# Kernel tuning notes

Measured on AMD Instinct MI355X. Metric: run time of the kernel, lower is better.

Reference implementation:

```python
import jax, jax.numpy as jnp
import numpy as np

N_NODES = 100000
N_EDGES = 1600000
D = 256
N_QUERY = 50000

def setup_inputs() -> dict:
    key = jax.random.key(0)
    k1, k2, k3, k4, k5, k6 = jax.random.split(key, 6)
    embeddings = jax.random.normal(k1, (N_NODES, D), dtype=jnp.float32)
    edge_src = jax.random.randint(k2, (N_EDGES,), 0, N_NODES)
    edge_dst = jax.random.randint(k3, (N_EDGES,), 0, N_NODES)
    edge_w = jax.random.uniform(k4, (N_EDGES,), dtype=jnp.float32)
    node_ids = jax.random.randint(k5, (N_QUERY,), 0, N_NODES)
    # Xavier-uniform linear weight, zero bias (as in _init_weights)
    limit = float(np.sqrt(6.0 / (D + D)))
    W = jax.random.uniform(k6, (D, D), dtype=jnp.float32, minval=-limit, maxval=limit)
    b = jnp.zeros((D,), dtype=jnp.float32)
    return {"embeddings": embeddings, "edge_src": edge_src, "edge_dst": edge_dst,
            "edge_w": edge_w, "node_ids": node_ids, "W": W, "b": b}

def reference(embeddings, edge_src, edge_dst, edge_w, node_ids, W, b):
    # graph_convolution: sparse adj (COO) @ embeddings == scatter-add of weighted src rows into dst
    msgs = embeddings[edge_src] * edge_w[:, None]                # [E, D]
    agg = jax.ops.segment_sum(msgs, edge_dst, num_segments=N_NODES)  # [N, D]
    # predict_scores: gather queried nodes, apply linear classifier
    feats = agg[node_ids]                                        # [Q, D]
    return feats @ W.T + b                                       # [Q, D]
```

## Files before the change

kernel.cpp:

```cpp
#include <hip/hip_runtime.h>

#define D 256
#define TQ 32
#define GQ 64

typedef __attribute__((ext_vector_type(8))) short short8;
typedef __attribute__((ext_vector_type(4))) float f32x4;

__device__ __forceinline__ unsigned short f2bf(float x) {
    unsigned int u = __float_as_uint(x);
    unsigned int r = (u + 0x7FFFu + ((u >> 16) & 1u)) >> 16;
    return (unsigned short)r;
}


__global__ __launch_bounds__(256) void flag_kernel(
    const int* __restrict__ nid, unsigned char* __restrict__ flags, int Q)
{
    int q = blockIdx.x * 256 + threadIdx.x;
    if (q < Q) flags[nid[q]] = 1;
}

__global__ __launch_bounds__(256) void hist_kernel(
    const int* __restrict__ edst, const unsigned char* __restrict__ flags,
    int* __restrict__ counts, int E)
{
    int stride = gridDim.x * 256;
    for (int e = blockIdx.x * 256 + threadIdx.x; e < E; e += stride) {
        int d = edst[e];
        if (flags[d]) atomicAdd(&counts[d], 1);
    }
}

__global__ __launch_bounds__(256) void alloc_kernel(
    const int* __restrict__ counts, int* __restrict__ base,
    int* __restrict__ pos, int* __restrict__ total, int N)
{
    int n = blockIdx.x * 256 + threadIdx.x;
    if (n >= N) return;
    int c = counts[n];
    int b = 0;
    if (c > 0) b = atomicAdd(total, c);
    base[n] = b;
    pos[n]  = b;
}

__global__ __launch_bounds__(256) void bucket_kernel(
    const int* __restrict__ esrc, const int* __restrict__ edst,
    const float* __restrict__ ew, const unsigned char* __restrict__ flags,
    int* __restrict__ pos, int2* __restrict__ bucket, int E)
{
    int stride = gridDim.x * 256;
    for (int e = blockIdx.x * 256 + threadIdx.x; e < E; e += stride) {
        int d = edst[e];
        if (flags[d]) {
            int idx = atomicAdd(&pos[d], 1);
            bucket[idx] = make_int2(esrc[e], __float_as_int(ew[e]));
        }
    }
}

__global__ __launch_bounds__(256) void accum_nodes(
    const float4* __restrict__ emb,
    const int2*   __restrict__ bucket,
    const int*    __restrict__ base,
    const int*    __restrict__ counts,
    const unsigned char* __restrict__ flags,
    float4*       __restrict__ agg,
    int N)
{
    const int lane = threadIdx.x & 63;
    const int wid  = (int)((blockIdx.x * 256 + threadIdx.x) >> 6);
    if (wid >= N) return;
    if (!flags[wid]) return;

    const int b = base[wid];
    const int c = counts[wid];
    float4 acc = make_float4(0.f, 0.f, 0.f, 0.f);

    int i = 0;
    for (; i + 4 <= c; i += 4) {
        int2 s0 = bucket[b + i + 0];
        int2 s1 = bucket[b + i + 1];
        int2 s2 = bucket[b + i + 2];
        int2 s3 = bucket[b + i + 3];
        float4 v0 = emb[(size_t)s0.x * (D / 4) + lane];
        float4 v1 = emb[(size_t)s1.x * (D / 4) + lane];
        float4 v2 = emb[(size_t)s2.x * (D / 4) + lane];
        float4 v3 = emb[(size_t)s3.x * (D / 4) + lane];
        float w0 = __int_as_float(s0.y), w1 = __int_as_float(s1.y);
        float w2 = __int_as_float(s2.y), w3 = __int_as_float(s3.y);
        acc.x += v0.x * w0; acc.y += v0.y * w0; acc.z += v0.z * w0; acc.w += v0.w * w0;
        acc.x += v1.x * w1; acc.y += v1.y * w1; acc.z += v1.z * w1; acc.w += v1.w * w1;
        acc.x += v2.x * w2; acc.y += v2.y * w2; acc.z += v2.z * w2; acc.w += v2.w * w2;
        acc.x += v3.x * w3; acc.y += v3.y * w3; acc.z += v3.z * w3; acc.w += v3.w * w3;
    }
    for (; i < c; ++i) {
        int2 s = bucket[b + i];
        float4 v = emb[(size_t)s.x * (D / 4) + lane];
        float w = __int_as_float(s.y);
        acc.x += v.x * w; acc.y += v.y * w; acc.z += v.z * w; acc.w += v.w * w;
    }
    agg[(size_t)wid * (D / 4) + lane] = acc;
}


__global__ __launch_bounds__(256) void scatter_edges(
    const float4* __restrict__ emb, const int* __restrict__ esrc,
    const int* __restrict__ edst, const float* __restrict__ ew,
    float* __restrict__ agg, int E)
{
    const int lane = threadIdx.x & 63;
    const int wid  = (int)((blockIdx.x * blockDim.x + threadIdx.x) >> 6);
    const int nw   = (int)((gridDim.x * blockDim.x) >> 6);
    for (int e = wid; e < E; e += nw) {
        const int   s = esrc[e];
        const int   d = edst[e];
        const float w = ew[e];
        float4 v = emb[(size_t)s * (D / 4) + lane];
        float* o = agg + (size_t)d * D + lane * 4;
        unsafeAtomicAdd(o + 0, v.x * w);
        unsafeAtomicAdd(o + 1, v.y * w);
        unsafeAtomicAdd(o + 2, v.z * w);
        unsafeAtomicAdd(o + 3, v.w * w);
    }
}

__global__ __launch_bounds__(256) void convert_w(
    const float* __restrict__ W, unsigned short* __restrict__ Wbf)
{
    int i = blockIdx.x * 256 + threadIdx.x;
    const float4* src = (const float4*)W + (size_t)i * 2;
    float4 v0 = src[0];
    float4 v1 = src[1];
    short8 p;
    p[0] = (short)f2bf(v0.x); p[1] = (short)f2bf(v0.y);
    p[2] = (short)f2bf(v0.z); p[3] = (short)f2bf(v0.w);
    p[4] = (short)f2bf(v1.x); p[5] = (short)f2bf(v1.y);
    p[6] = (short)f2bf(v1.z); p[7] = (short)f2bf(v1.w);
    *((short8*)Wbf + i) = p;
}

__global__ __launch_bounds__(256) void gather_gemm_mfma(
    const float* __restrict__ agg, const int* __restrict__ nid,
    const unsigned short* __restrict__ Wbf,
    const float* __restrict__ b,
    float* __restrict__ out, int Q)
{
    __shared__ unsigned char lds[GQ * 512];
    const int t  = threadIdx.x;
    const int q0 = blockIdx.x * GQ;

    #pragma unroll
    for (int s = 0; s < 8; ++s) {
        const int i   = t + s * 256;
        const int row = i >> 5;
        const int ch  = i & 31;
        const int q   = q0 + row;
        float4 v0 = make_float4(0.f, 0.f, 0.f, 0.f), v1 = v0;
        if (q < Q) {
            const float4* src = (const float4*)agg + (size_t)nid[q] * 64 + ch * 2;
            v0 = src[0];
            v1 = src[1];
        }
        short8 p;
        p[0] = (short)f2bf(v0.x); p[1] = (short)f2bf(v0.y);
        p[2] = (short)f2bf(v0.z); p[3] = (short)f2bf(v0.w);
        p[4] = (short)f2bf(v1.x); p[5] = (short)f2bf(v1.y);
        p[6] = (short)f2bf(v1.z); p[7] = (short)f2bf(v1.w);
        int byte = row * 512 + ch * 16;
        byte ^= (row & 7) << 4;
        *(short8*)(lds + byte) = p;
    }
    __syncthreads();

    const int wave = t >> 6;
    const int lane = t & 63;
    const int qw   = wave * 16;
    const int lrow = lane & 15;
    const int kg   = lane >> 4;

    short8 afrag[8];
    #pragma unroll
    for (int ks = 0; ks < 8; ++ks) {
        int byte = (qw + lrow) * 512 + ks * 64 + kg * 16;
        byte ^= ((qw + lrow) & 7) << 4;
        afrag[ks] = *(const short8*)(lds + byte);
    }

    const unsigned short* wp0 = Wbf + (size_t)lrow * 256 + kg * 8;

    for (int jt = 0; jt < 16; ++jt) {
        f32x4 acc = {0.f, 0.f, 0.f, 0.f};
        const unsigned short* wp = wp0 + (size_t)jt * 16 * 256;
        #pragma unroll
        for (int ks = 0; ks < 8; ++ks) {
            short8 bfrag = *(const short8*)(wp + ks * 32);
            acc = __builtin_amdgcn_mfma_f32_16x16x32_bf16(afrag[ks], bfrag, acc, 0, 0, 0);
        }
        const float bias = b[jt * 16 + lrow];
        #pragma unroll
        for (int r = 0; r < 4; ++r) {
            const int row = kg * 4 + r;
            const int q   = q0 + qw + row;
            if (q < Q) out[(size_t)q * D + jt * 16 + lrow] = acc[r] + bias;
        }
    }
}

__global__ __launch_bounds__(256) void gather_gemm_w(
    const float* __restrict__ agg, const int* __restrict__ nid,
    const float* __restrict__ W, const float* __restrict__ b,
    float* __restrict__ out, int Q)
{
    __shared__ float fl[TQ][D];
    const int t  = threadIdx.x;
    const int q0 = blockIdx.x * TQ;

    for (int i = t; i < TQ * (D / 4); i += 256) {
        const int r = i >> 6;
        const int c = i & 63;
        const int q = q0 + r;
        float4 v = make_float4(0.f, 0.f, 0.f, 0.f);
        if (q < Q) v = ((const float4*)agg)[(size_t)nid[q] * (D / 4) + c];
        ((float4*)&fl[r][0])[c] = v;
    }
    __syncthreads();

    const int j = t;
    float acc[TQ];
    #pragma unroll
    for (int r = 0; r < TQ; ++r) acc[r] = 0.f;

    const float4* wr4 = (const float4*)(W + (size_t)j * D);
    for (int k4 = 0; k4 < D / 4; ++k4) {
        const float4 w4 = wr4[k4];
        #pragma unroll
        for (int r = 0; r < TQ; ++r) {
            const float4 f = ((const float4*)&fl[r][0])[k4];
            acc[r] += f.x * w4.x + f.y * w4.y + f.z * w4.z + f.w * w4.w;
        }
    }

    const float bias = b[j];
    #pragma unroll
    for (int r = 0; r < TQ; ++r) {
        const int q = q0 + r;
        if (q < Q) out[(size_t)q * D + j] = acc[r] + bias;
    }
}

extern "C" void kernel_launch(void* const* d_in, const int* in_sizes, int n_in,
                              void* d_out, int out_size, void* d_ws, size_t ws_size,
                              hipStream_t stream) {
    const float* emb  = (const float*)d_in[0];
    const int*   esrc = (const int*)d_in[1];
    const int*   edst = (const int*)d_in[2];
    const float* ew   = (const float*)d_in[3];
    const int*   nid  = (const int*)d_in[4];
    const float* W    = (const float*)d_in[5];
    const float* b    = (const float*)d_in[6];
    float*       out  = (float*)d_out;

    const int N = in_sizes[0] / D;
    const int E = in_sizes[1];
    const int Q = in_sizes[4];

    char* wsb = (char*)d_ws;

    size_t off_agg    = 0;
    size_t off_counts = off_agg    + (size_t)N * D * sizeof(float);
    size_t off_base   = off_counts + (size_t)N * sizeof(int);
    size_t off_pos    = off_base   + (size_t)N * sizeof(int);
    size_t off_total  = off_pos    + (size_t)N * sizeof(int);
    size_t off_flags  = off_total  + 256;
    size_t off_bucket = off_flags  + (((size_t)N + 255) / 256) * 256;
    size_t off_wbf    = off_bucket + (size_t)E * sizeof(int2);
    size_t needed     = off_wbf    + (size_t)D * D * sizeof(unsigned short);

    float*          agg = (float*)(wsb + off_agg);
    unsigned short* Wbf = (unsigned short*)(wsb + off_wbf);

    const bool big_ws = (ws_size >= needed);

    if (big_ws) {
        int*           counts = (int*)(wsb + off_counts);
        int*           basep  = (int*)(wsb + off_base);
        int*           pos    = (int*)(wsb + off_pos);
        int*           total  = (int*)(wsb + off_total);
        unsigned char* flags  = (unsigned char*)(wsb + off_flags);
        int2*          bucket = (int2*)(wsb + off_bucket);

        hipMemsetAsync(wsb + off_counts, 0, off_bucket - off_counts, stream);

        convert_w    <<<32, 256, 0, stream>>>(W, Wbf);
        flag_kernel  <<<(Q + 255) / 256, 256, 0, stream>>>(nid, flags, Q);
        hist_kernel  <<<2048, 256, 0, stream>>>(edst, flags, counts, E);
        alloc_kernel <<<(N + 255) / 256, 256, 0, stream>>>(counts, basep, pos, total, N);
        bucket_kernel<<<2048, 256, 0, stream>>>(esrc, edst, ew, flags, pos, bucket, E);

        int nb_acc = (int)(((size_t)N * 64 + 255) / 256);
        accum_nodes<<<nb_acc, 256, 0, stream>>>((const float4*)emb, bucket, basep,
                                                counts, flags, (float4*)agg, N);

        const int nb = (Q + GQ - 1) / GQ;
        gather_gemm_mfma<<<nb, 256, 0, stream>>>(agg, nid, Wbf, b, out, Q);
    } else {
        hipMemsetAsync(agg, 0, (size_t)N * D * sizeof(float), stream);
        scatter_edges<<<2048, 256, 0, stream>>>((const float4*)emb, esrc, edst, ew, agg, E);
        const int nb = (Q + TQ - 1) / TQ;
        gather_gemm_w<<<nb, 256, 0, stream>>>(agg, nid, W, b, out, Q);
    }
}
```

Baseline: 405.7 us.

## Gather bf16 embeddings, store bf16 aggregate, and use LDS bitmask for query flags

```diff
diff --git a/kernel.cpp b/kernel.cpp
--- a/kernel.cpp
+++ b/kernel.cpp
@@ -3,8 +3,10 @@
 #define D 256
 #define TQ 32
 #define GQ 64
+#define NBW 3136
 
 typedef __attribute__((ext_vector_type(8))) short short8;
+typedef __attribute__((ext_vector_type(4))) short short4v;
 typedef __attribute__((ext_vector_type(4))) float f32x4;
 
 __device__ __forceinline__ unsigned short f2bf(float x) {
@@ -12,23 +14,64 @@
     unsigned int r = (u + 0x7FFFu + ((u >> 16) & 1u)) >> 16;
     return (unsigned short)r;
 }
-
-
-__global__ __launch_bounds__(256) void flag_kernel(
-    const int* __restrict__ nid, unsigned char* __restrict__ flags, int Q)
+__device__ __forceinline__ float bf2f(unsigned short h) {
+    return __uint_as_float(((unsigned int)h) << 16);
+}
+
+
+__global__ __launch_bounds__(256) void convert_emb(
+    const float4* __restrict__ emb, short8* __restrict__ embbf, int total8)
+{
+    int stride = gridDim.x * 256;
+    for (int i = blockIdx.x * 256 + threadIdx.x; i < total8; i += stride) {
+        float4 v0 = emb[(size_t)i * 2 + 0];
+        float4 v1 = emb[(size_t)i * 2 + 1];
+        short8 p;
+        p[0] = (short)f2bf(v0.x); p[1] = (short)f2bf(v0.y);
+        p[2] = (short)f2bf(v0.z); p[3] = (short)f2bf(v0.w);
+        p[4] = (short)f2bf(v1.x); p[5] = (short)f2bf(v1.y);
+        p[6] = (short)f2bf(v1.z); p[7] = (short)f2bf(v1.w);
+        embbf[i] = p;
+    }
+}
+
+__global__ __launch_bounds__(256) void convert_w(
+    const float* __restrict__ W, unsigned short* __restrict__ Wbf)
+{
+    int i = blockIdx.x * 256 + threadIdx.x;
+    const float4* src = (const float4*)W + (size_t)i * 2;
+    float4 v0 = src[0];
+    float4 v1 = src[1];
+    short8 p;
+    p[0] = (short)f2bf(v0.x); p[1] = (short)f2bf(v0.y);
+    p[2] = (short)f2bf(v0.z); p[3] = (short)f2bf(v0.w);
+    p[4] = (short)f2bf(v1.x); p[5] = (short)f2bf(v1.y);
+    p[6] = (short)f2bf(v1.z); p[7] = (short)f2bf(v1.w);
+    *((short8*)Wbf + i) = p;
+}
+
+
+__global__ __launch_bounds__(256) void flag_bits(
+    const int* __restrict__ nid, unsigned int* __restrict__ bits, int Q)
 {
     int q = blockIdx.x * 256 + threadIdx.x;
-    if (q < Q) flags[nid[q]] = 1;
+    if (q < Q) {
+        int v = nid[q];
+        atomicOr(&bits[v >> 5], 1u << (v & 31));
+    }
 }
 
 __global__ __launch_bounds__(256) void hist_kernel(
-    const int* __restrict__ edst, const unsigned char* __restrict__ flags,
+    const int* __restrict__ edst, const unsigned int* __restrict__ bits,
     int* __restrict__ counts, int E)
 {
+    __shared__ unsigned int lb[NBW];
+    for (int i = threadIdx.x; i < NBW; i += 256) lb[i] = bits[i];
+    __syncthreads();
     int stride = gridDim.x * 256;
     for (int e = blockIdx.x * 256 + threadIdx.x; e < E; e += stride) {
         int d = edst[e];
-        if (flags[d]) atomicAdd(&counts[d], 1);
+        if ((lb[d >> 5] >> (d & 31)) & 1u) atomicAdd(&counts[d], 1);
     }
 }
 
@@ -47,13 +90,16 @@
 
 __global__ __launch_bounds__(256) void bucket_kernel(
     const int* __restrict__ esrc, const int* __restrict__ edst,
-    const float* __restrict__ ew, const unsigned char* __restrict__ flags,
+    const float* __restrict__ ew, const unsigned int* __restrict__ bits,
     int* __restrict__ pos, int2* __restrict__ bucket, int E)
 {
+    __shared__ unsigned int lb[NBW];
+    for (int i = threadIdx.x; i < NBW; i += 256) lb[i] = bits[i];
+    __syncthreads();
     int stride = gridDim.x * 256;
     for (int e = blockIdx.x * 256 + threadIdx.x; e < E; e += stride) {
         int d = edst[e];
-        if (flags[d]) {
+        if ((lb[d >> 5] >> (d & 31)) & 1u) {
             int idx = atomicAdd(&pos[d], 1);
             bucket[idx] = make_int2(esrc[e], __float_as_int(ew[e]));
         }
@@ -61,47 +107,108 @@
 }
 
 __global__ __launch_bounds__(256) void accum_nodes(
-    const float4* __restrict__ emb,
-    const int2*   __restrict__ bucket,
-    const int*    __restrict__ base,
-    const int*    __restrict__ counts,
-    const unsigned char* __restrict__ flags,
-    float4*       __restrict__ agg,
+    const short4v* __restrict__ embbf,
+    const int2*    __restrict__ bucket,
+    const int*     __restrict__ base,
+    const int*     __restrict__ counts,
+    const unsigned int* __restrict__ bits,
+    short4v*       __restrict__ aggbf,
     int N)
 {
     const int lane = threadIdx.x & 63;
     const int wid  = (int)((blockIdx.x * 256 + threadIdx.x) >> 6);
     if (wid >= N) return;
-    if (!flags[wid]) return;
+    if (!((bits[wid >> 5] >> (wid & 31)) & 1u)) return;
 
     const int b = base[wid];
     const int c = counts[wid];
-    float4 acc = make_float4(0.f, 0.f, 0.f, 0.f);
+    float a0 = 0.f, a1 = 0.f, a2 = 0.f, a3 = 0.f;
 
     int i = 0;
-    for (; i + 4 <= c; i += 4) {
-        int2 s0 = bucket[b + i + 0];
-        int2 s1 = bucket[b + i + 1];
-        int2 s2 = bucket[b + i + 2];
-        int2 s3 = bucket[b + i + 3];
-        float4 v0 = emb[(size_t)s0.x * (D / 4) + lane];
-        float4 v1 = emb[(size_t)s1.x * (D / 4) + lane];
-        float4 v2 = emb[(size_t)s2.x * (D / 4) + lane];
-        float4 v3 = emb[(size_t)s3.x * (D / 4) + lane];
-        float w0 = __int_as_float(s0.y), w1 = __int_as_float(s1.y);
-        float w2 = __int_as_float(s2.y), w3 = __int_as_float(s3.y);
-        acc.x += v0.x * w0; acc.y += v0.y * w0; acc.z += v0.z * w0; acc.w += v0.w * w0;
-        acc.x += v1.x * w1; acc.y += v1.y * w1; acc.z += v1.z * w1; acc.w += v1.w * w1;
-        acc.x += v2.x * w2; acc.y += v2.y * w2; acc.z += v2.z * w2; acc.w += v2.w * w2;
-        acc.x += v3.x * w3; acc.y += v3.y * w3; acc.z += v3.z * w3; acc.w += v3.w * w3;
+    for (; i + 8 <= c; i += 8) {
+        #pragma unroll
+        for (int u = 0; u < 8; ++u) {
+            int2 s = bucket[b + i + u];
+            short4v v = embbf[(size_t)s.x * 64 + lane];
+            float w = __int_as_float(s.y);
+            a0 += bf2f((unsigned short)v[0]) * w;
+            a1 += bf2f((unsigned short)v[1]) * w;
+            a2 += bf2f((unsigned short)v[2]) * w;
+            a3 += bf2f((unsigned short)v[3]) * w;
+        }
     }
     for (; i < c; ++i) {
         int2 s = bucket[b + i];
-        float4 v = emb[(size_t)s.x * (D / 4) + lane];
+        short4v v = embbf[(size_t)s.x * 64 + lane];
         float w = __int_as_float(s.y);
-        acc.x += v.x * w; acc.y += v.y * w; acc.z += v.z * w; acc.w += v.w * w;
-    }
-    agg[(size_t)wid * (D / 4) + lane] = acc;
+        a0 += bf2f((unsigned short)v[0]) * w;
+        a1 += bf2f((unsigned short)v[1]) * w;
+        a2 += bf2f((unsigned short)v[2]) * w;
+        a3 += bf2f((unsigned short)v[3]) * w;
+    }
+    short4v o;
+    o[0] = (short)f2bf(a0); o[1] = (short)f2bf(a1);
+    o[2] = (short)f2bf(a2); o[3] = (short)f2bf(a3);
+    aggbf[(size_t)wid * 64 + lane] = o;
+}
+
+__global__ __launch_bounds__(256) void gather_gemm_mfma(
+    const unsigned short* __restrict__ aggbf,
+    const int* __restrict__ nid,
+    const unsigned short* __restrict__ Wbf,
+    const float* __restrict__ b,
+    float* __restrict__ out, int Q)
+{
+    __shared__ unsigned char lds[GQ * 512];
+    const int t  = threadIdx.x;
+    const int q0 = blockIdx.x * GQ;
+
+    #pragma unroll
+    for (int s = 0; s < 8; ++s) {
+        const int i   = t + s * 256;
+        const int row = i >> 5;
+        const int ch  = i & 31;
+        const int q   = q0 + row;
+        short8 p = {0, 0, 0, 0, 0, 0, 0, 0};
+        if (q < Q) p = *((const short8*)aggbf + (size_t)nid[q] * 32 + ch);
+        int byte = row * 512 + ch * 16;
+        byte ^= (row & 7) << 4;
+        *(short8*)(lds + byte) = p;
+    }
+    __syncthreads();
+
+    const int wave = t >> 6;
+    const int lane = t & 63;
+    const int qw   = wave * 16;
+    const int lrow = lane & 15;
+    const int kg   = lane >> 4;
+
+    short8 afrag[8];
+    #pragma unroll
+    for (int ks = 0; ks < 8; ++ks) {
+        int byte = (qw + lrow) * 512 + ks * 64 + kg * 16;
+        byte ^= ((qw + lrow) & 7) << 4;
+        afrag[ks] = *(const short8*)(lds + byte);
+    }
+
+    const unsigned short* wp0 = Wbf + (size_t)lrow * 256 + kg * 8;
+
+    for (int jt = 0; jt < 16; ++jt) {
+        f32x4 acc = {0.f, 0.f, 0.f, 0.f};
+        const unsigned short* wp = wp0 + (size_t)jt * 16 * 256;
+        #pragma unroll
+        for (int ks = 0; ks < 8; ++ks) {
+            short8 bfrag = *(const short8*)(wp + ks * 32);
+            acc = __builtin_amdgcn_mfma_f32_16x16x32_bf16(afrag[ks], bfrag, acc, 0, 0, 0);
+        }
+        const float bias = b[jt * 16 + lrow];
+        #pragma unroll
+        for (int r = 0; r < 4; ++r) {
+            const int row = kg * 4 + r;
+            const int q   = q0 + qw + row;
+            if (q < Q) out[(size_t)q * D + jt * 16 + lrow] = acc[r] + bias;
+        }
+    }
 }
 
 
@@ -126,88 +233,6 @@
     }
 }
 
-__global__ __launch_bounds__(256) void convert_w(
-    const float* __restrict__ W, unsigned short* __restrict__ Wbf)
-{
-    int i = blockIdx.x * 256 + threadIdx.x;
-    const float4* src = (const float4*)W + (size_t)i * 2;
-    float4 v0 = src[0];
-    float4 v1 = src[1];
-    short8 p;
-    p[0] = (short)f2bf(v0.x); p[1] = (short)f2bf(v0.y);
-    p[2] = (short)f2bf(v0.z); p[3] = (short)f2bf(v0.w);
-    p[4] = (short)f2bf(v1.x); p[5] = (short)f2bf(v1.y);
-    p[6] = (short)f2bf(v1.z); p[7] = (short)f2bf(v1.w);
-    *((short8*)Wbf + i) = p;
-}
-
-__global__ __launch_bounds__(256) void gather_gemm_mfma(
-    const float* __restrict__ agg, const int* __restrict__ nid,
-    const unsigned short* __restrict__ Wbf,
-    const float* __restrict__ b,
-    float* __restrict__ out, int Q)
-{
-    __shared__ unsigned char lds[GQ * 512];
-    const int t  = threadIdx.x;
-    const int q0 = blockIdx.x * GQ;
-
-    #pragma unroll
-    for (int s = 0; s < 8; ++s) {
-        const int i   = t + s * 256;
-        const int row = i >> 5;
-        const int ch  = i & 31;
-        const int q   = q0 + row;
-        float4 v0 = make_float4(0.f, 0.f, 0.f, 0.f), v1 = v0;
-        if (q < Q) {
-            const float4* src = (const float4*)agg + (size_t)nid[q] * 64 + ch * 2;
-            v0 = src[0];
-            v1 = src[1];
-        }
-        short8 p;
-        p[0] = (short)f2bf(v0.x); p[1] = (short)f2bf(v0.y);
-        p[2] = (short)f2bf(v0.z); p[3] = (short)f2bf(v0.w);
-        p[4] = (short)f2bf(v1.x); p[5] = (short)f2bf(v1.y);
-        p[6] = (short)f2bf(v1.z); p[7] = (short)f2bf(v1.w);
-        int byte = row * 512 + ch * 16;
-        byte ^= (row & 7) << 4;
-        *(short8*)(lds + byte) = p;
-    }
-    __syncthreads();
-
-    const int wave = t >> 6;
-    const int lane = t & 63;
-    const int qw   = wave * 16;
-    const int lrow = lane & 15;
-    const int kg   = lane >> 4;
-
-    short8 afrag[8];
-    #pragma unroll
-    for (int ks = 0; ks < 8; ++ks) {
-        int byte = (qw + lrow) * 512 + ks * 64 + kg * 16;
-        byte ^= ((qw + lrow) & 7) << 4;
-        afrag[ks] = *(const short8*)(lds + byte);
-    }
-
-    const unsigned short* wp0 = Wbf + (size_t)lrow * 256 + kg * 8;
-
-    for (int jt = 0; jt < 16; ++jt) {
-        f32x4 acc = {0.f, 0.f, 0.f, 0.f};
-        const unsigned short* wp = wp0 + (size_t)jt * 16 * 256;
-        #pragma unroll
-        for (int ks = 0; ks < 8; ++ks) {
-            short8 bfrag = *(const short8*)(wp + ks * 32);
-            acc = __builtin_amdgcn_mfma_f32_16x16x32_bf16(afrag[ks], bfrag, acc, 0, 0, 0);
-        }
-        const float bias = b[jt * 16 + lrow];
-        #pragma unroll
-        for (int r = 0; r < 4; ++r) {
-            const int row = kg * 4 + r;
-            const int q   = q0 + qw + row;
-            if (q < Q) out[(size_t)q * D + jt * 16 + lrow] = acc[r] + bias;
-        }
-    }
-}
-
 __global__ __launch_bounds__(256) void gather_gemm_w(
     const float* __restrict__ agg, const int* __restrict__ nid,
     const float* __restrict__ W, const float* __restrict__ b,
@@ -269,43 +294,44 @@
     char* wsb = (char*)d_ws;
 
     size_t off_agg    = 0;
-    size_t off_counts = off_agg    + (size_t)N * D * sizeof(float);
+    size_t off_emb    = off_agg    + (size_t)N * D * 2;
+    size_t off_counts = off_emb    + (size_t)N * D * 2;
     size_t off_base   = off_counts + (size_t)N * sizeof(int);
     size_t off_pos    = off_base   + (size_t)N * sizeof(int);
     size_t off_total  = off_pos    + (size_t)N * sizeof(int);
-    size_t off_flags  = off_total  + 256;
-    size_t off_bucket = off_flags  + (((size_t)N + 255) / 256) * 256;
+    size_t off_bits   = off_total  + 256;
+    size_t off_bucket = off_bits   + (size_t)NBW * 4;
     size_t off_wbf    = off_bucket + (size_t)E * sizeof(int2);
-    size_t needed     = off_wbf    + (size_t)D * D * sizeof(unsigned short);
-
-    float*          agg = (float*)(wsb + off_agg);
-    unsigned short* Wbf = (unsigned short*)(wsb + off_wbf);
-
-    const bool big_ws = (ws_size >= needed);
-
-    if (big_ws) {
-        int*           counts = (int*)(wsb + off_counts);
-        int*           basep  = (int*)(wsb + off_base);
-        int*           pos    = (int*)(wsb + off_pos);
-        int*           total  = (int*)(wsb + off_total);
-        unsigned char* flags  = (unsigned char*)(wsb + off_flags);
-        int2*          bucket = (int2*)(wsb + off_bucket);
+    size_t needed     = off_wbf    + (size_t)D * D * 2;
+
+    if (ws_size >= needed) {
+        unsigned short* aggbf  = (unsigned short*)(wsb + off_agg);
+        short8*         embbf  = (short8*)(wsb + off_emb);
+        int*            counts = (int*)(wsb + off_counts);
+        int*            basep  = (int*)(wsb + off_base);
+        int*            pos    = (int*)(wsb + off_pos);
+        int*            total  = (int*)(wsb + off_total);
+        unsigned int*   bits   = (unsigned int*)(wsb + off_bits);
+        int2*           bucket = (int2*)(wsb + off_bucket);
+        unsigned short* Wbf    = (unsigned short*)(wsb + off_wbf);
 
         hipMemsetAsync(wsb + off_counts, 0, off_bucket - off_counts, stream);
 
+        convert_emb  <<<2048, 256, 0, stream>>>((const float4*)emb, embbf, N * D / 8);
         convert_w    <<<32, 256, 0, stream>>>(W, Wbf);
-        flag_kernel  <<<(Q + 255) / 256, 256, 0, stream>>>(nid, flags, Q);
-        hist_kernel  <<<2048, 256, 0, stream>>>(edst, flags, counts, E);
+        flag_bits    <<<(Q + 255) / 256, 256, 0, stream>>>(nid, bits, Q);
+        hist_kernel  <<<2048, 256, 0, stream>>>(edst, bits, counts, E);
         alloc_kernel <<<(N + 255) / 256, 256, 0, stream>>>(counts, basep, pos, total, N);
-        bucket_kernel<<<2048, 256, 0, stream>>>(esrc, edst, ew, flags, pos, bucket, E);
+        bucket_kernel<<<2048, 256, 0, stream>>>(esrc, edst, ew, bits, pos, bucket, E);
 
         int nb_acc = (int)(((size_t)N * 64 + 255) / 256);
-        accum_nodes<<<nb_acc, 256, 0, stream>>>((const float4*)emb, bucket, basep,
-                                                counts, flags, (float4*)agg, N);
+        accum_nodes<<<nb_acc, 256, 0, stream>>>((const short4v*)embbf, bucket, basep,
+                                                counts, bits, (short4v*)aggbf, N);
 
         const int nb = (Q + GQ - 1) / GQ;
-        gather_gemm_mfma<<<nb, 256, 0, stream>>>(agg, nid, Wbf, b, out, Q);
+        gather_gemm_mfma<<<nb, 256, 0, stream>>>(aggbf, nid, Wbf, b, out, Q);
     } else {
+        float* agg = (float*)wsb;
         hipMemsetAsync(agg, 0, (size_t)N * D * sizeof(float), stream);
         scatter_edges<<<2048, 256, 0, stream>>>((const float4*)emb, esrc, edst, ew, agg, E);
         const int nb = (Q + TQ - 1) / TQ;
```

New measurement: 402.8 us. About the same (-0.7%).
